# Performance work log

Hardware: AMD Instinct MI355X
Metric: run time of the kernel (lower is better)

Reference implementation:

```python
import jax, jax.numpy as jnp
import numpy as np


def setup_inputs() -> dict:
    key = jax.random.key(0)
    k1, k2 = jax.random.split(key)
    N1, N2 = 16384, 16384
    pos1 = jax.random.normal(k1, (N1, 2), dtype=jnp.float32)
    pos2 = jax.random.normal(k2, (N2, 2), dtype=jnp.float32)
    return {"pos1": pos1, "pos2": pos2}


def reference(pos1, pos2):
    # pos1: [N1, 2], pos2: [N2, 2]
    diff = pos1[:, None, :] - pos2[None, :, :]          # [N1, N2, 2]
    dist = jnp.sqrt(jnp.sum(diff * diff, axis=2))       # [N1, N2]
    nearest = jnp.min(dist, axis=1)                     # [N1]
    return jnp.mean(nearest)
```

## Files before the change

### kernel.cpp

```cpp
#include <hip/hip_runtime.h>
#include <math.h>

#define N1 16384
#define N2 16384
#define BLOCK 512
#define PTS 4
#define I_BLOCKS (N1 / (BLOCK * PTS))
#define SLICES 128
#define SLICE_F4 ((N2 / SLICES) / 2)
#define FBLOCK 256

__device__ __forceinline__ unsigned int f2key(float f) {
    unsigned int b = __float_as_uint(f);
    return (b & 0x80000000u) ? ~b : (b | 0x80000000u);
}
__device__ __forceinline__ float key2f(unsigned int k) {
    unsigned int b = (k & 0x80000000u) ? (k & 0x7FFFFFFFu) : ~k;
    return __uint_as_float(b);
}

__global__ __launch_bounds__(BLOCK, 8)
void nn_partial(const float2* __restrict__ pos1,
                const float4* __restrict__ pos2,
                unsigned int* __restrict__ keys,
                unsigned int* __restrict__ ticket,
                int slice_f4) {
    const int ib = blockIdx.x;
    const int sl = blockIdx.y;
    const int t  = threadIdx.x;

    if (ib == 0 && sl == 0 && t == 0) *ticket = 0;

    const float4* __restrict__ q = pos2 + (size_t)sl * slice_f4;
    const int i0 = ib * (BLOCK * PTS) + t;

    float x[PTS], y[PTS], m[PTS];
#pragma unroll
    for (int k = 0; k < PTS; ++k) {
        float2 p = pos1[i0 + k * BLOCK];
        x[k] = -2.f * p.x;
        y[k] = -2.f * p.y;
        m[k] = 3.4e38f;
    }

#pragma unroll 4
    for (int j = 0; j < slice_f4; ++j) {
        float4 qq = q[j];
        float az = fmaf(qq.x, qq.x, qq.y * qq.y);
        float bz = fmaf(qq.z, qq.z, qq.w * qq.w);
#pragma unroll
        for (int k = 0; k < PTS; ++k) {
            float ta = fmaf(x[k], qq.x, fmaf(y[k], qq.y, az));
            float tb = fmaf(x[k], qq.z, fmaf(y[k], qq.w, bz));
            m[k] = fminf(m[k], fminf(ta, tb));
        }
    }

#pragma unroll
    for (int k = 0; k < PTS; ++k) {
        atomicMin(&keys[i0 + k * BLOCK], f2key(m[k]));
    }
}

__global__ __launch_bounds__(FBLOCK)
void nn_finish(const unsigned int* __restrict__ keys,
               const float2* __restrict__ pos1,
               float* __restrict__ blocksums,
               unsigned int* __restrict__ ticket,
               float* __restrict__ out) {
    const int t = threadIdx.x;
    const int i = blockIdx.x * FBLOCK + t;

    float g = key2f(keys[i]);
    float2 p = pos1[i];
    float d2 = fmaxf(fmaf(p.x, p.x, p.y * p.y) + g, 0.f);
    float sum = sqrtf(d2);

    for (int off = 32; off > 0; off >>= 1) {
        sum += __shfl_down(sum, off, 64);
    }
    __shared__ float wsum[FBLOCK / 64];
    __shared__ int lastflag;
    if ((t & 63) == 0) wsum[t >> 6] = sum;
    __syncthreads();
    if (t == 0) {
        float s = 0.f;
        for (int w = 0; w < FBLOCK / 64; ++w) s += wsum[w];
        blocksums[blockIdx.x] = s;
        __threadfence();
        unsigned int old = atomicAdd(ticket, 1u);
        lastflag = (old == gridDim.x - 1) ? 1 : 0;
    }
    __syncthreads();
    if (lastflag && t < 64) {
        volatile float* vb = (volatile float*)blocksums;
        float v = vb[t];
        for (int off = 32; off > 0; off >>= 1) {
            v += __shfl_down(v, off, 64);
        }
        if (t == 0) out[0] = v / (float)N1;
    }
}

extern "C" void kernel_launch(void* const* d_in, const int* in_sizes, int n_in,
                              void* d_out, int out_size, void* d_ws, size_t ws_size,
                              hipStream_t stream) {
    const float2* pos1 = (const float2*)d_in[0];
    const float4* pos2 = (const float4*)d_in[1];
    float* out = (float*)d_out;

    unsigned int* keys = (unsigned int*)d_ws;
    float* blocksums   = (float*)(keys + N1);
    unsigned int* ticket = (unsigned int*)(blocksums + 64);

    const int slice_f4 = (N2 / SLICES) / 2;

    hipMemsetAsync(keys, 0xFF, (size_t)N1 * sizeof(unsigned int), stream);

    dim3 grid1(I_BLOCKS, SLICES);
    nn_partial<<<grid1, BLOCK, 0, stream>>>(pos1, pos2, keys, ticket, slice_f4);
    nn_finish<<<N1 / FBLOCK, FBLOCK, 0, stream>>>(keys, pos1, blocksums, ticket, out);
}
```

Baseline: 80.91 us.

## Replace atomicMin keys with per-slice partial buffer reduced in finish kernel

Each slice block now writes its per-point minima into a dense partials array instead of doing atomicMin on order-preserving integer keys, and the finish kernel takes the min across slices. This removes the memset launch and global atomics. Slice count is halved so the partial buffer stays small, and the slice length becomes a compile-time constant. The costs are a 4 MB write and read of partials and a grid half as large, with longer per-block loops in the first kernel.

```diff
diff --git a/kernel.cpp b/kernel.cpp
--- a/kernel.cpp
+++ b/kernel.cpp
@@ -6,32 +6,21 @@
 #define BLOCK 512
 #define PTS 4
 #define I_BLOCKS (N1 / (BLOCK * PTS))
-#define SLICES 128
+#define SLICES 64
 #define SLICE_F4 ((N2 / SLICES) / 2)
 #define FBLOCK 256
-
-__device__ __forceinline__ unsigned int f2key(float f) {
-    unsigned int b = __float_as_uint(f);
-    return (b & 0x80000000u) ? ~b : (b | 0x80000000u);
-}
-__device__ __forceinline__ float key2f(unsigned int k) {
-    unsigned int b = (k & 0x80000000u) ? (k & 0x7FFFFFFFu) : ~k;
-    return __uint_as_float(b);
-}
 
 __global__ __launch_bounds__(BLOCK, 8)
 void nn_partial(const float2* __restrict__ pos1,
                 const float4* __restrict__ pos2,
-                unsigned int* __restrict__ keys,
-                unsigned int* __restrict__ ticket,
-                int slice_f4) {
+                float* __restrict__ partials,
+                unsigned int* __restrict__ ticket) {
     const int ib = blockIdx.x;
     const int sl = blockIdx.y;
     const int t  = threadIdx.x;
 
     if (ib == 0 && sl == 0 && t == 0) *ticket = 0;
-
-    const float4* __restrict__ q = pos2 + (size_t)sl * slice_f4;
+    const float4* __restrict__ q = pos2 + (size_t)sl * SLICE_F4;
     const int i0 = ib * (BLOCK * PTS) + t;
 
     float x[PTS], y[PTS], m[PTS];
@@ -44,7 +33,7 @@
     }
 
 #pragma unroll 4
-    for (int j = 0; j < slice_f4; ++j) {
+    for (int j = 0; j < SLICE_F4; ++j) {
         float4 qq = q[j];
         float az = fmaf(qq.x, qq.x, qq.y * qq.y);
         float bz = fmaf(qq.z, qq.z, qq.w * qq.w);
@@ -56,14 +45,15 @@
         }
     }
 
+    float* dst = partials + (size_t)sl * N1 + i0;
 #pragma unroll
     for (int k = 0; k < PTS; ++k) {
-        atomicMin(&keys[i0 + k * BLOCK], f2key(m[k]));
+        dst[k * BLOCK] = m[k];
     }
 }
 
 __global__ __launch_bounds__(FBLOCK)
-void nn_finish(const unsigned int* __restrict__ keys,
+void nn_finish(const float* __restrict__ partials,
                const float2* __restrict__ pos1,
                float* __restrict__ blocksums,
                unsigned int* __restrict__ ticket,
@@ -71,7 +61,12 @@
     const int t = threadIdx.x;
     const int i = blockIdx.x * FBLOCK + t;
 
-    float g = key2f(keys[i]);
+    float g = 3.4e38f;
+#pragma unroll 8
+    for (int sl = 0; sl < SLICES; ++sl) {
+        g = fminf(g, partials[(size_t)sl * N1 + i]);
+    }
+
     float2 p = pos1[i];
     float d2 = fmaxf(fmaf(p.x, p.x, p.y * p.y) + g, 0.f);
     float sum = sqrtf(d2);
@@ -109,15 +104,12 @@
     const float4* pos2 = (const float4*)d_in[1];
     float* out = (float*)d_out;
 
-    unsigned int* keys = (unsigned int*)d_ws;
-    float* blocksums   = (float*)(keys + N1);
+    float* partials      = (float*)d_ws;
+    float* blocksums     = partials + (size_t)SLICES * N1;
     unsigned int* ticket = (unsigned int*)(blocksums + 64);
 
-    const int slice_f4 = (N2 / SLICES) / 2;
-
-    hipMemsetAsync(keys, 0xFF, (size_t)N1 * sizeof(unsigned int), stream);
-
     dim3 grid1(I_BLOCKS, SLICES);
-    nn_partial<<<grid1, BLOCK, 0, stream>>>(pos1, pos2, keys, ticket, slice_f4);
-    nn_finish<<<N1 / FBLOCK, FBLOCK, 0, stream>>>(keys, pos1, blocksums, ticket, out);
+    nn_partial<<<grid1, BLOCK, 0, stream>>>(pos1, pos2, partials, ticket);
+    nn_finish<<<N1 / FBLOCK, FBLOCK, 0, stream>>>(partials, pos1, blocksums,
+                                                  ticket, out);
 }
```

After: 91.67 us. +13.3%, slower.
